# Optimization experiments

Measured on AMD Instinct MI355X. Metric: run time of the kernel, lower is better.

Reference implementation:

```python
import jax, jax.numpy as jnp
import numpy as np

N_CLASSES = 10
NBD_PAD = 1
EPS = 1e-5  # nn.LayerNorm default eps


def _neighbor_states(state, n):
    # state: [B, n_classes, H, W]; replicates F.unfold(kernel=2n+1, padding=n)
    # then drops the center tap. Kernel positions enumerated row-major, matching
    # unfold's (C, K2) channel ordering after the view in the torch code.
    B, C, H, W = state.shape
    k = 2 * n + 1
    center = (k * k) // 2
    padded = jnp.pad(state, ((0, 0), (0, 0), (n, n), (n, n)))
    shifts = []
    for idx in range(k * k):
        if idx == center:
            continue
        ki, kj = divmod(idx, k)
        shifts.append(padded[:, :, ki:ki + H, kj:kj + W])
    nb = jnp.stack(shifts, axis=2)  # [B, C, K2-1, H, W]
    return nb.reshape(B, C * (k * k - 1), H, W)


def setup_inputs() -> dict:
    key = jax.random.key(0)
    ks = jax.random.split(key, 7)
    B, C, H, W = 64, 32, 128, 128
    NN_HID, PERC = 128, 112
    x = jax.random.normal(ks[0], (B, C, H, W), dtype=jnp.float32)
    w1 = jax.random.normal(ks[1], (NN_HID, PERC), dtype=jnp.float32) * (1.0 / np.sqrt(PERC))
    b1 = jax.random.normal(ks[2], (NN_HID,), dtype=jnp.float32) * 0.02
    w2 = jax.random.normal(ks[3], (C, NN_HID), dtype=jnp.float32) * (1.0 / np.sqrt(NN_HID))
    b2 = jax.random.normal(ks[4], (C,), dtype=jnp.float32) * 0.02
    gamma = jnp.ones((C,), dtype=jnp.float32) + 0.1 * jax.random.normal(ks[5], (C,), dtype=jnp.float32)
    beta = 0.1 * jax.random.normal(ks[6], (C,), dtype=jnp.float32)
    return {"x": x, "w1": w1, "b1": b1, "w2": w2, "b2": b2, "gamma": gamma, "beta": beta}


def reference(x, w1, b1, w2, b2, gamma, beta):
    # perceive: [B, in_ch + n_classes*(K2-1), H, W]
    nb = _neighbor_states(x[:, :N_CLASSES], NBD_PAD)
    perc = jnp.concatenate([x, nb], axis=1)
    # 1x1 conv MLP (fire_rate == 1.0 -> no update mask)
    h = jax.nn.relu(jnp.einsum('bchw,oc->bohw', perc, w1) + b1[None, :, None, None])
    dx = jnp.einsum('bchw,oc->bohw', h, w2) + b2[None, :, None, None]
    new_state = x + dx
    # clean_slate_if_white: zero hidden channels where argmax class == 0 (no_grad mask)
    pred = jnp.argmax(new_state[:, :N_CLASSES], axis=1)  # [B,H,W]
    inv = jax.lax.stop_gradient((pred != 0).astype(new_state.dtype))[:, None]  # [B,1,H,W]
    new_state = jnp.concatenate(
        [new_state[:, :N_CLASSES], new_state[:, N_CLASSES:] * inv], axis=1)
    # LayerNorm over channel dim (torch permutes to NHWC, norms last dim, permutes back)
    mu = jnp.mean(new_state, axis=1, keepdims=True)
    var = jnp.var(new_state, axis=1, keepdims=True)
    xn = (new_state - mu) * jax.lax.rsqrt(var + EPS)
    return xn * gamma[None, :, None, None] + beta[None, :, None, None]
```

## Files before the change

kernel.cpp:

```cpp
#include <hip/hip_runtime.h>

typedef unsigned short U16;
typedef unsigned int U32;
typedef __bf16 bf16;
typedef bf16 bf16x8 __attribute__((ext_vector_type(8)));
typedef U16  u16x8  __attribute__((ext_vector_type(8)));
typedef float f32x4 __attribute__((ext_vector_type(4)));

__device__ __forceinline__ void split3(float a, U16& o1, U16& o2, U16& o3) {
    U32 ua = __float_as_uint(a);
    float a1 = __uint_as_float(ua & 0xFFFF0000u);
    float r1 = a - a1;
    U32 u2 = __float_as_uint(r1);
    float a2 = __uint_as_float(u2 & 0xFFFF0000u);
    float r2 = r1 - a2;
    o1 = (U16)(ua >> 16);
    o2 = (U16)(u2 >> 16);
    o3 = (U16)(__float_as_uint(r2) >> 16);
}

__device__ __forceinline__ void split3x8(const float v[8], bf16x8& A1, bf16x8& A2, bf16x8& A3) {
    u16x8 e1, e2, e3;
    #pragma unroll
    for (int j = 0; j < 8; ++j) { U16 a, b, c; split3(v[j], a, b, c); e1[j] = a; e2[j] = b; e3[j] = c; }
    A1 = __builtin_bit_cast(bf16x8, e1);
    A2 = __builtin_bit_cast(bf16x8, e2);
    A3 = __builtin_bit_cast(bf16x8, e3);
}

__global__ __launch_bounds__(256)
void prep_kernel(const float* __restrict__ w1g, const float* __restrict__ w2g,
                 U16* __restrict__ w1L, U16* __restrict__ w2L)
{
    int tid = blockIdx.x * 256 + threadIdx.x;
    if (tid < 2048) {
        int n = tid >> 4, k0 = (tid & 15) << 3;
        float v[8];
        #pragma unroll
        for (int j = 0; j < 8; ++j) { int k = k0 + j; v[j] = (k < 112) ? w1g[n * 112 + k] : 0.0f; }
        bf16x8 L1, L2, L3; split3x8(v, L1, L2, L3);
        *(bf16x8*)(w1L + 0 * 16384 + n * 128 + k0) = L1;
        *(bf16x8*)(w1L + 1 * 16384 + n * 128 + k0) = L2;
        *(bf16x8*)(w1L + 2 * 16384 + n * 128 + k0) = L3;
    }
    if (tid < 512) {
        int n = tid >> 4, k0 = (tid & 15) << 3;
        float v[8];
        #pragma unroll
        for (int j = 0; j < 8; ++j) v[j] = w2g[n * 128 + k0 + j];
        bf16x8 L1, L2, L3; split3x8(v, L1, L2, L3);
        *(bf16x8*)(w2L + 0 * 4096 + n * 128 + k0) = L1;
        *(bf16x8*)(w2L + 1 * 4096 + n * 128 + k0) = L2;
        *(bf16x8*)(w2L + 2 * 4096 + n * 128 + k0) = L3;
    }
}

#define WBAR() do { asm volatile("s_waitcnt lgkmcnt(0)" ::: "memory"); \
                    __builtin_amdgcn_s_barrier();                      \
                    asm volatile("" ::: "memory"); } while (0)
#define RBAR() do { asm volatile("" ::: "memory");                     \
                    __builtin_amdgcn_s_barrier();                      \
                    asm volatile("" ::: "memory"); } while (0)

__device__ __forceinline__ void tap_load(const float* __restrict__ xg, int b, int irow,
                                         int jbase, int j, float v[8])
{
    int tpx = j & 63, cls = j >> 6;
    const float* cbase = xg + (b * 32 + cls) * 16384;
    #pragma unroll
    for (int t = 0; t < 8; ++t) {
        int di = (int)((0x22211000u >> (4 * t)) & 0xFu) - 1;
        int dj = (int)((0x21020210u >> (4 * t)) & 0xFu) - 1;
        int row = irow + di;
        int cc  = jbase + tpx + dj;
        bool okb = ((unsigned)row < 128u) && ((unsigned)cc < 128u);
        int off = okb ? (row * 128 + cc) : 0;
        float x = cbase[off];
        v[t] = okb ? x : 0.0f;
    }
}

__device__ __forceinline__ void tap_write(U16* sL, int j, const float v[8])
{
    int tpx = j & 63, cls = j >> 6;
    bf16x8 T1, T2, T3; split3x8(v, T1, T2, T3);
    int to = tpx * 136 + 32 + cls * 8;
    *(bf16x8*)&sL[to] = T1;
    *(bf16x8*)&sL[8704 + to] = T2;
    *(bf16x8*)&sL[17408 + to] = T3;
}

#define LDW1(g, ks_) do {                                                    \
    _Pragma("unroll") for (int L_ = 0; L_ < 3; ++L_)                         \
    _Pragma("unroll") for (int n_ = 0; n_ < 2; ++n_)                         \
        g[L_ * 2 + n_] = *(const bf16x8*)(w1p + L_ * 16384 + n_ * 2048 + (ks_) * 32); \
} while (0)

#define MFMA1(ks_, g) do {                                                   \
    _Pragma("unroll") for (int mt_ = 0; mt_ < 4; ++mt_) {                    \
        const int ao_ = (mt_ * 16 + col) * 136 + (ks_) * 32 + quad * 8;      \
        bf16x8 A1_ = *(const bf16x8*)&sL[ao_];                               \
        bf16x8 A2_ = *(const bf16x8*)&sL[8704 + ao_];                        \
        bf16x8 A3_ = *(const bf16x8*)&sL[17408 + ao_];                       \
        _Pragma("unroll") for (int n_ = 0; n_ < 2; ++n_) {                   \
            f32x4 a_ = acc1[mt_][n_];                                        \
            a_ = __builtin_amdgcn_mfma_f32_16x16x32_bf16(A1_, g[0 + n_], a_, 0, 0, 0); \
            a_ = __builtin_amdgcn_mfma_f32_16x16x32_bf16(A1_, g[2 + n_], a_, 0, 0, 0); \
            a_ = __builtin_amdgcn_mfma_f32_16x16x32_bf16(A2_, g[0 + n_], a_, 0, 0, 0); \
            a_ = __builtin_amdgcn_mfma_f32_16x16x32_bf16(A1_, g[4 + n_], a_, 0, 0, 0); \
            a_ = __builtin_amdgcn_mfma_f32_16x16x32_bf16(A2_, g[2 + n_], a_, 0, 0, 0); \
            a_ = __builtin_amdgcn_mfma_f32_16x16x32_bf16(A3_, g[0 + n_], a_, 0, 0, 0); \
            acc1[mt_][n_] = a_;                                              \
        }                                                                    \
    }                                                                        \
} while (0)

#define LDW2(q, ks_) do {                                                    \
    _Pragma("unroll") for (int L_ = 0; L_ < 3; ++L_)                         \
    _Pragma("unroll") for (int n_ = 0; n_ < 2; ++n_)                         \
        q[L_ * 2 + n_] = *(const bf16x8*)(w2p + L_ * 4096 + n_ * 2048 + (ks_) * 32); \
} while (0)

#define MFMA2(ks_, q) do {                                                   \
    const int ho_ = (wv * 16 + col) * 136 + (ks_) * 32 + quad * 8;           \
    bf16x8 H1_ = *(const bf16x8*)&sL[ho_];                                   \
    bf16x8 H2_ = *(const bf16x8*)&sL[8704 + ho_];                            \
    bf16x8 H3_ = *(const bf16x8*)&sL[17408 + ho_];                           \
    _Pragma("unroll") for (int n_ = 0; n_ < 2; ++n_) {                       \
        f32x4 a_ = acc2[n_];                                                 \
        a_ = __builtin_amdgcn_mfma_f32_16x16x32_bf16(H1_, q[0 + n_], a_, 0, 0, 0); \
        a_ = __builtin_amdgcn_mfma_f32_16x16x32_bf16(H1_, q[2 + n_], a_, 0, 0, 0); \
        a_ = __builtin_amdgcn_mfma_f32_16x16x32_bf16(H2_, q[0 + n_], a_, 0, 0, 0); \
        a_ = __builtin_amdgcn_mfma_f32_16x16x32_bf16(H1_, q[4 + n_], a_, 0, 0, 0); \
        a_ = __builtin_amdgcn_mfma_f32_16x16x32_bf16(H2_, q[2 + n_], a_, 0, 0, 0); \
        a_ = __builtin_amdgcn_mfma_f32_16x16x32_bf16(H3_, q[0 + n_], a_, 0, 0, 0); \
        acc2[n_] = a_;                                                       \
    }                                                                        \
} while (0)

__global__ __launch_bounds__(256, 3)
void cann_kernel(const float* __restrict__ xg,  const U16* __restrict__ w1L,
                 const U16* __restrict__ w2L,
                 const float* __restrict__ b1g, const float* __restrict__ b2g,
                 const float* __restrict__ gg,  const float* __restrict__ bg,
                 float* __restrict__ outg)
{
    __shared__ __align__(16) U16 sL[3 * 8704];

    const int tid  = threadIdx.x;
    const int bid0 = blockIdx.x;
    const int bid  = (bid0 & 7) * 2048 + (bid0 >> 3);
    const int jseg = bid & 1;
    const int irow = (bid >> 1) & 127;
    const int b    = bid >> 8;
    const int jbase = jseg << 6;
    const int lane = tid & 63;
    const int wv   = tid >> 6;
    const int quad = lane >> 4;
    const int col  = lane & 15;
    const int px   = tid & 63;
    const int cg   = tid >> 6;

    const U16* w1p = w1L + (wv * 32 + col) * 128 + quad * 8;
    const U16* w2p = w2L + col * 128 + quad * 8;

    {
        const float* src = xg + (b * 32 + cg * 8) * 16384 + irow * 128 + jbase + px;
        float va[8];
        #pragma unroll
        for (int i = 0; i < 8; ++i) va[i] = src[i * 16384];
        bf16x8 L1, L2, L3; split3x8(va, L1, L2, L3);
        int o = px * 136 + cg * 8;
        *(bf16x8*)&sL[o] = L1;
        *(bf16x8*)&sL[8704 + o] = L2;
        *(bf16x8*)&sL[17408 + o] = L3;
    }
    {
        float vt[8];
        tap_load(xg, b, irow, jbase, tid, vt);       tap_write(sL, tid, vt);
        tap_load(xg, b, irow, jbase, tid + 256, vt); tap_write(sL, tid + 256, vt);
        if (tid < 128) { tap_load(xg, b, irow, jbase, tid + 512, vt);
                         tap_write(sL, tid + 512, vt); }
    }
    if (tid < 128) {
        int zo = (tid >> 1) * 136 + 112 + (tid & 1) * 8;
        uint4 z = make_uint4(0u, 0u, 0u, 0u);
        *(uint4*)&sL[zo] = z;
        *(uint4*)&sL[8704 + zo] = z;
        *(uint4*)&sL[17408 + zo] = z;
    }

    const float b1v0 = b1g[wv * 32 + col];
    const float b1v1 = b1g[wv * 32 + 16 + col];
    const float b2v0 = b2g[col];
    const float b2v1 = b2g[16 + col];
    float xs[2][4];
    #pragma unroll
    for (int n2 = 0; n2 < 2; ++n2)
        #pragma unroll
        for (int r = 0; r < 4; ++r)
            xs[n2][r] = xg[(b * 32 + n2 * 16 + col) * 16384 + irow * 128 + jbase
                           + wv * 16 + quad * 4 + r];

    bf16x8 g0[6], g1[6], g2[6], g3[6];
    LDW1(g0, 0);
    LDW1(g1, 1);

    WBAR();

    const f32x4 fz = {0.f, 0.f, 0.f, 0.f};
    f32x4 acc1[4][2];
    #pragma unroll
    for (int mt = 0; mt < 4; ++mt) { acc1[mt][0] = fz; acc1[mt][1] = fz; }

    LDW1(g2, 2);
    __builtin_amdgcn_sched_group_barrier(0x20, 6, 0);
    MFMA1(0, g0);
    LDW1(g3, 3);
    __builtin_amdgcn_sched_group_barrier(0x20, 6, 0);
    MFMA1(1, g1);
    MFMA1(2, g2);
    MFMA1(3, g3);

    RBAR();

    bf16x8 q0[6], q1[6], q2[6], q3[6];
    LDW2(q0, 0);
    LDW2(q1, 1);
    __builtin_amdgcn_sched_group_barrier(0x20, 12, 0);

    #pragma unroll
    for (int mt = 0; mt < 4; ++mt)
        #pragma unroll
        for (int n2 = 0; n2 < 2; ++n2) {
            float bb = n2 ? b1v1 : b1v0;
            #pragma unroll
            for (int r = 0; r < 4; ++r) {
                float v = fmaxf(acc1[mt][n2][r] + bb, 0.0f);
                U16 u1, u2, u3; split3(v, u1, u2, u3);
                int ho = (mt * 16 + quad * 4 + r) * 136 + wv * 32 + n2 * 16 + col;
                sL[ho] = u1; sL[8704 + ho] = u2; sL[17408 + ho] = u3;
            }
        }

    WBAR();

    f32x4 acc2[2];
    acc2[0] = fz; acc2[1] = fz;

    LDW2(q2, 2);
    __builtin_amdgcn_sched_group_barrier(0x20, 6, 0);
    MFMA2(0, q0);
    LDW2(q3, 3);
    __builtin_amdgcn_sched_group_barrier(0x20, 6, 0);
    MFMA2(1, q1);
    MFMA2(2, q2);
    MFMA2(3, q3);

    RBAR();

    float* dxl = (float*)sL;
    #pragma unroll
    for (int n2 = 0; n2 < 2; ++n2) {
        float bb = n2 ? b2v1 : b2v0;
        int c = n2 * 16 + col;
        #pragma unroll
        for (int r = 0; r < 4; ++r) {
            int p = wv * 16 + quad * 4 + r;
            dxl[p * 33 + c] = acc2[n2][r] + bb + xs[n2][r];
        }
    }

    WBAR();

    if (tid < 64) {
        int p = tid;
        float ns[32];
        #pragma unroll
        for (int c = 0; c < 32; ++c) ns[c] = dxl[p * 33 + c];
        float m = ns[1];
        #pragma unroll
        for (int c = 2; c < 10; ++c) m = fmaxf(m, ns[c]);
        float keep = (m > ns[0]) ? 1.0f : 0.0f;
        #pragma unroll
        for (int c = 10; c < 32; ++c) ns[c] *= keep;
        float s = 0.f;
        #pragma unroll
        for (int c = 0; c < 32; ++c) s += ns[c];
        float mu = s * 0.03125f;
        float var = 0.f;
        #pragma unroll
        for (int c = 0; c < 32; ++c) { float d = ns[c] - mu; var += d * d; }
        var *= 0.03125f;
        float rstd = 1.0f / sqrtf(var + 1e-5f);
        int base = b * 524288 + irow * 128 + jbase + p;
        #pragma unroll
        for (int c = 0; c < 32; ++c)
            outg[base + c * 16384] = (ns[c] - mu) * rstd * gg[c] + bg[c];
    }
}

extern "C" void kernel_launch(void* const* d_in, const int* in_sizes, int n_in,
                              void* d_out, int out_size, void* d_ws, size_t ws_size,
                              hipStream_t stream) {
    const float* x  = (const float*)d_in[0];
    const float* w1 = (const float*)d_in[1];
    const float* b1 = (const float*)d_in[2];
    const float* w2 = (const float*)d_in[3];
    const float* b2 = (const float*)d_in[4];
    const float* g  = (const float*)d_in[5];
    const float* be = (const float*)d_in[6];
    float* out = (float*)d_out;

    U16* w1L = (U16*)d_ws;
    U16* w2L = (U16*)((char*)d_ws + 98304);

    hipLaunchKernelGGL(prep_kernel, dim3(8), dim3(256), 0, stream, w1, w2, w1L, w2L);
    hipLaunchKernelGGL(cann_kernel, dim3(16384), dim3(256), 0, stream,
                       x, w1L, w2L, b1, b2, g, be, out);
}
```

Measured before the change: 578.0 us.

## Process two 64-pixel tiles per block and prefetch the second tile's inputs

Each block now handles a full 128-pixel row as two tiles, halving the grid. The global loads for the second tile are issued during the first tile's second GEMM so their latency overlaps compute. The MFMA operands are swapped, which transposes the accumulator layout and allows vectorized u16x4 stores of the hidden activations and f32x4 stores into a padded dx buffer. In exchange the prefetch buffers raise register pressure, and the grid has less parallelism to hide latency.

```diff
diff --git a/kernel.cpp b/kernel.cpp
--- a/kernel.cpp
+++ b/kernel.cpp
@@ -5,6 +5,7 @@
 typedef __bf16 bf16;
 typedef bf16 bf16x8 __attribute__((ext_vector_type(8)));
 typedef U16  u16x8  __attribute__((ext_vector_type(8)));
+typedef U16  u16x4  __attribute__((ext_vector_type(4)));
 typedef float f32x4 __attribute__((ext_vector_type(4)));
 
 __device__ __forceinline__ void split3(float a, U16& o1, U16& o2, U16& o3) {
@@ -90,13 +91,62 @@
     *(bf16x8*)&sL[17408 + to] = T3;
 }
 
+__device__ __forceinline__ void load_tile(const float* __restrict__ xg, int b, int irow,
+                                          int jbase, int tid, int px, int cg,
+                                          int wv, int quad, int col,
+                                          float va[8], float vt0[8], float vt1[8],
+                                          float vt2[8], float xs[2][4])
+{
+    const float* src = xg + (b * 32 + cg * 8) * 16384 + irow * 128 + jbase + px;
+    #pragma unroll
+    for (int i = 0; i < 8; ++i) va[i] = src[i * 16384];
+    tap_load(xg, b, irow, jbase, tid,       vt0);
+    tap_load(xg, b, irow, jbase, tid + 256, vt1);
+    if (tid < 128) tap_load(xg, b, irow, jbase, tid + 512, vt2);
+    #pragma unroll
+    for (int n2 = 0; n2 < 2; ++n2)
+        #pragma unroll
+        for (int r = 0; r < 4; ++r)
+            xs[n2][r] = xg[(b * 32 + n2 * 16 + quad * 4 + r) * 16384
+                           + irow * 128 + jbase + wv * 16 + col];
+}
+
+__device__ __forceinline__ void stage_all(U16* sL, int tid, int px, int cg,
+                                          const float va[8], const float vt0[8],
+                                          const float vt1[8], const float vt2[8])
+{
+    {
+        bf16x8 L1, L2, L3; split3x8(va, L1, L2, L3);
+        int o = px * 136 + cg * 8;
+        *(bf16x8*)&sL[o] = L1;
+        *(bf16x8*)&sL[8704 + o] = L2;
+        *(bf16x8*)&sL[17408 + o] = L3;
+    }
+    tap_write(sL, tid,       vt0);
+    tap_write(sL, tid + 256, vt1);
+    if (tid < 128) tap_write(sL, tid + 512, vt2);
+    if (tid < 128) {
+        int zo = (tid >> 1) * 136 + 112 + (tid & 1) * 8;
+        uint4 z = make_uint4(0u, 0u, 0u, 0u);
+        *(uint4*)&sL[zo] = z;
+        *(uint4*)&sL[8704 + zo] = z;
+        *(uint4*)&sL[17408 + zo] = z;
+    }
+}
+
 #define LDW1(g, ks_) do {                                                    \
     _Pragma("unroll") for (int L_ = 0; L_ < 3; ++L_)                         \
     _Pragma("unroll") for (int n_ = 0; n_ < 2; ++n_)                         \
         g[L_ * 2 + n_] = *(const bf16x8*)(w1p + L_ * 16384 + n_ * 2048 + (ks_) * 32); \
 } while (0)
 
-#define MFMA1(ks_, g) do {                                                   \
+#define LDW2(q, ks_) do {                                                    \
+    _Pragma("unroll") for (int L_ = 0; L_ < 3; ++L_)                         \
+    _Pragma("unroll") for (int n_ = 0; n_ < 2; ++n_)                         \
+        q[L_ * 2 + n_] = *(const bf16x8*)(w2p + L_ * 4096 + n_ * 2048 + (ks_) * 32); \
+} while (0)
+
+#define MFMA1S(ks_, g) do {                                                  \
     _Pragma("unroll") for (int mt_ = 0; mt_ < 4; ++mt_) {                    \
         const int ao_ = (mt_ * 16 + col) * 136 + (ks_) * 32 + quad * 8;      \
         bf16x8 A1_ = *(const bf16x8*)&sL[ao_];                               \
@@ -104,38 +154,149 @@
         bf16x8 A3_ = *(const bf16x8*)&sL[17408 + ao_];                       \
         _Pragma("unroll") for (int n_ = 0; n_ < 2; ++n_) {                   \
             f32x4 a_ = acc1[mt_][n_];                                        \
-            a_ = __builtin_amdgcn_mfma_f32_16x16x32_bf16(A1_, g[0 + n_], a_, 0, 0, 0); \
-            a_ = __builtin_amdgcn_mfma_f32_16x16x32_bf16(A1_, g[2 + n_], a_, 0, 0, 0); \
-            a_ = __builtin_amdgcn_mfma_f32_16x16x32_bf16(A2_, g[0 + n_], a_, 0, 0, 0); \
-            a_ = __builtin_amdgcn_mfma_f32_16x16x32_bf16(A1_, g[4 + n_], a_, 0, 0, 0); \
-            a_ = __builtin_amdgcn_mfma_f32_16x16x32_bf16(A2_, g[2 + n_], a_, 0, 0, 0); \
-            a_ = __builtin_amdgcn_mfma_f32_16x16x32_bf16(A3_, g[0 + n_], a_, 0, 0, 0); \
+            a_ = __builtin_amdgcn_mfma_f32_16x16x32_bf16(g[0 + n_], A1_, a_, 0, 0, 0); \
+            a_ = __builtin_amdgcn_mfma_f32_16x16x32_bf16(g[2 + n_], A1_, a_, 0, 0, 0); \
+            a_ = __builtin_amdgcn_mfma_f32_16x16x32_bf16(g[0 + n_], A2_, a_, 0, 0, 0); \
+            a_ = __builtin_amdgcn_mfma_f32_16x16x32_bf16(g[4 + n_], A1_, a_, 0, 0, 0); \
+            a_ = __builtin_amdgcn_mfma_f32_16x16x32_bf16(g[2 + n_], A2_, a_, 0, 0, 0); \
+            a_ = __builtin_amdgcn_mfma_f32_16x16x32_bf16(g[0 + n_], A3_, a_, 0, 0, 0); \
             acc1[mt_][n_] = a_;                                              \
         }                                                                    \
     }                                                                        \
 } while (0)
 
-#define LDW2(q, ks_) do {                                                    \
-    _Pragma("unroll") for (int L_ = 0; L_ < 3; ++L_)                         \
-    _Pragma("unroll") for (int n_ = 0; n_ < 2; ++n_)                         \
-        q[L_ * 2 + n_] = *(const bf16x8*)(w2p + L_ * 4096 + n_ * 2048 + (ks_) * 32); \
-} while (0)
-
-#define MFMA2(ks_, q) do {                                                   \
+#define MFMA2S(ks_, q) do {                                                  \
     const int ho_ = (wv * 16 + col) * 136 + (ks_) * 32 + quad * 8;           \
     bf16x8 H1_ = *(const bf16x8*)&sL[ho_];                                   \
     bf16x8 H2_ = *(const bf16x8*)&sL[8704 + ho_];                            \
     bf16x8 H3_ = *(const bf16x8*)&sL[17408 + ho_];                           \
     _Pragma("unroll") for (int n_ = 0; n_ < 2; ++n_) {                       \
         f32x4 a_ = acc2[n_];                                                 \
-        a_ = __builtin_amdgcn_mfma_f32_16x16x32_bf16(H1_, q[0 + n_], a_, 0, 0, 0); \
-        a_ = __builtin_amdgcn_mfma_f32_16x16x32_bf16(H1_, q[2 + n_], a_, 0, 0, 0); \
-        a_ = __builtin_amdgcn_mfma_f32_16x16x32_bf16(H2_, q[0 + n_], a_, 0, 0, 0); \
-        a_ = __builtin_amdgcn_mfma_f32_16x16x32_bf16(H1_, q[4 + n_], a_, 0, 0, 0); \
-        a_ = __builtin_amdgcn_mfma_f32_16x16x32_bf16(H2_, q[2 + n_], a_, 0, 0, 0); \
-        a_ = __builtin_amdgcn_mfma_f32_16x16x32_bf16(H3_, q[0 + n_], a_, 0, 0, 0); \
+        a_ = __builtin_amdgcn_mfma_f32_16x16x32_bf16(q[0 + n_], H1_, a_, 0, 0, 0); \
+        a_ = __builtin_amdgcn_mfma_f32_16x16x32_bf16(q[2 + n_], H1_, a_, 0, 0, 0); \
+        a_ = __builtin_amdgcn_mfma_f32_16x16x32_bf16(q[0 + n_], H2_, a_, 0, 0, 0); \
+        a_ = __builtin_amdgcn_mfma_f32_16x16x32_bf16(q[4 + n_], H1_, a_, 0, 0, 0); \
+        a_ = __builtin_amdgcn_mfma_f32_16x16x32_bf16(q[2 + n_], H2_, a_, 0, 0, 0); \
+        a_ = __builtin_amdgcn_mfma_f32_16x16x32_bf16(q[0 + n_], H3_, a_, 0, 0, 0); \
         acc2[n_] = a_;                                                       \
     }                                                                        \
+} while (0)
+
+#define EPI3(jb_) do {                                                       \
+    const float* dxr_ = (const float*)sL;                                    \
+    int p_ = tid;                                                            \
+    f32x4 e0_ = *(const f32x4*)&dxr_[p_ * 36 + 0];                           \
+    f32x4 e1_ = *(const f32x4*)&dxr_[p_ * 36 + 4];                           \
+    f32x4 e2_ = *(const f32x4*)&dxr_[p_ * 36 + 8];                           \
+    float m_ = e0_[1];                                                       \
+    m_ = fmaxf(m_, e0_[2]); m_ = fmaxf(m_, e0_[3]);                          \
+    m_ = fmaxf(m_, e1_[0]); m_ = fmaxf(m_, e1_[1]);                          \
+    m_ = fmaxf(m_, e1_[2]); m_ = fmaxf(m_, e1_[3]);                          \
+    m_ = fmaxf(m_, e2_[0]); m_ = fmaxf(m_, e2_[1]);                          \
+    float keep_ = (m_ > e0_[0]) ? 1.0f : 0.0f;                               \
+    float s_ = 0.f;                                                          \
+    s_ += e0_[0]; s_ += e0_[1]; s_ += e0_[2]; s_ += e0_[3];                  \
+    s_ += e1_[0]; s_ += e1_[1]; s_ += e1_[2]; s_ += e1_[3];                  \
+    s_ += e2_[0]; s_ += e2_[1];                                              \
+    s_ += e2_[2] * keep_; s_ += e2_[3] * keep_;                              \
+    _Pragma("unroll")                                                        \
+    for (int i_ = 3; i_ < 8; ++i_) {                                         \
+        f32x4 v_ = *(const f32x4*)&dxr_[p_ * 36 + i_ * 4];                   \
+        s_ += v_[0] * keep_; s_ += v_[1] * keep_;                            \
+        s_ += v_[2] * keep_; s_ += v_[3] * keep_;                            \
+    }                                                                        \
+    float mu_ = s_ * 0.03125f;                                               \
+    float var_ = 0.f;                                                        \
+    _Pragma("unroll")                                                        \
+    for (int i_ = 0; i_ < 8; ++i_) {                                         \
+        f32x4 v_ = *(const f32x4*)&dxr_[p_ * 36 + i_ * 4];                   \
+        _Pragma("unroll")                                                    \
+        for (int j_ = 0; j_ < 4; ++j_) {                                     \
+            int c_ = i_ * 4 + j_;                                            \
+            float x_ = (c_ >= 10) ? v_[j_] * keep_ : v_[j_];                 \
+            float d_ = x_ - mu_; var_ += d_ * d_;                            \
+        }                                                                    \
+    }                                                                        \
+    var_ *= 0.03125f;                                                        \
+    float rstd_ = 1.0f / sqrtf(var_ + 1e-5f);                                \
+    int base_ = b * 524288 + irow * 128 + (jb_) + p_;                        \
+    _Pragma("unroll")                                                        \
+    for (int i_ = 0; i_ < 8; ++i_) {                                         \
+        f32x4 v_ = *(const f32x4*)&dxr_[p_ * 36 + i_ * 4];                   \
+        _Pragma("unroll")                                                    \
+        for (int j_ = 0; j_ < 4; ++j_) {                                     \
+            int c_ = i_ * 4 + j_;                                            \
+            float x_ = (c_ >= 10) ? v_[j_] * keep_ : v_[j_];                 \
+            outg[base_ + c_ * 16384] = (x_ - mu_) * rstd_ * gg[c_] + bg[c_]; \
+        }                                                                    \
+    }                                                                        \
+} while (0)
+
+#define TILE_BODY(jb_, XS_, PRE_, jb2_, XSN_) do {                           \
+    stage_all(sL, tid, px, cg, va, vt0, vt1, vt2);                           \
+    bf16x8 g0[6], g1[6], g2[6], g3[6];                                       \
+    LDW1(g0, 0); LDW1(g1, 1);                                                \
+    WBAR();             \
+    f32x4 acc1[4][2];                                                        \
+    _Pragma("unroll")                                                        \
+    for (int mt_ = 0; mt_ < 4; ++mt_) { acc1[mt_][0] = fz; acc1[mt_][1] = fz; } \
+    LDW1(g2, 2);                                                             \
+    __builtin_amdgcn_sched_group_barrier(0x20, 6, 0);                        \
+    MFMA1S(0, g0);                                                           \
+    LDW1(g3, 3);                                                             \
+    __builtin_amdgcn_sched_group_barrier(0x20, 6, 0);                        \
+    MFMA1S(1, g1);                                                           \
+    MFMA1S(2, g2);                                                           \
+    MFMA1S(3, g3);                                                           \
+    RBAR();            \
+    bf16x8 q0[6], q1[6], q2[6], q3[6];                                       \
+    LDW2(q0, 0); LDW2(q1, 1);                                                \
+    __builtin_amdgcn_sched_group_barrier(0x20, 12, 0);                       \
+     \
+    _Pragma("unroll")                                                        \
+    for (int mt_ = 0; mt_ < 4; ++mt_)                                        \
+        _Pragma("unroll")                                                    \
+        for (int n_ = 0; n_ < 2; ++n_) {                                     \
+            u16x4 o1_, o2_, o3_;                                             \
+            _Pragma("unroll")                                                \
+            for (int r_ = 0; r_ < 4; ++r_) {                                 \
+                float v_ = fmaxf(acc1[mt_][n_][r_] + b1v[n_][r_], 0.0f);     \
+                U16 u1_, u2_, u3_; split3(v_, u1_, u2_, u3_);                \
+                o1_[r_] = u1_; o2_[r_] = u2_; o3_[r_] = u3_;                 \
+            }                                                                \
+            int ho_ = (mt_ * 16 + col) * 136 + wv * 32 + n_ * 16 + quad * 4; \
+            *(u16x4*)&sL[ho_] = o1_;                                         \
+            *(u16x4*)&sL[8704 + ho_] = o2_;                                  \
+            *(u16x4*)&sL[17408 + ho_] = o3_;                                 \
+        }                                                                    \
+    WBAR();                                      \
+    if (PRE_) load_tile(xg, b, irow, (jb2_), tid, px, cg, wv, quad, col,     \
+                        va, vt0, vt1, vt2, XSN_);                            \
+    f32x4 acc2[2];                                                           \
+    acc2[0] = fz; acc2[1] = fz;                                              \
+    LDW2(q2, 2);                                                             \
+    __builtin_amdgcn_sched_group_barrier(0x20, 6, 0);                        \
+    MFMA2S(0, q0);                                                           \
+    LDW2(q3, 3);                                                             \
+    __builtin_amdgcn_sched_group_barrier(0x20, 6, 0);                        \
+    MFMA2S(1, q1);                                                           \
+    MFMA2S(2, q2);                                                           \
+    MFMA2S(3, q3);                                                           \
+    RBAR();         \
+    {        \
+        float* dxl_ = (float*)sL;                                            \
+        _Pragma("unroll")                                                    \
+        for (int n_ = 0; n_ < 2; ++n_) {                                     \
+            f32x4 vv_;                                                       \
+            _Pragma("unroll")                                                \
+            for (int r_ = 0; r_ < 4; ++r_)                                   \
+                vv_[r_] = acc2[n_][r_] + b2v[n_][r_] + XS_[n_][r_];          \
+            *(f32x4*)&dxl_[(wv * 16 + col) * 36 + n_ * 16 + quad * 4] = vv_; \
+        }                                                                    \
+    }                                                                        \
+    WBAR();                                      \
+    if (tid < 64) EPI3(jb_);                                                 \
+    if (PRE_) WBAR();   \
 } while (0)
 
 __global__ __launch_bounds__(256, 3)
@@ -149,11 +310,9 @@
 
     const int tid  = threadIdx.x;
     const int bid0 = blockIdx.x;
-    const int bid  = (bid0 & 7) * 2048 + (bid0 >> 3);
-    const int jseg = bid & 1;
-    const int irow = (bid >> 1) & 127;
-    const int b    = bid >> 8;
-    const int jbase = jseg << 6;
+    const int bid  = (bid0 & 7) * 1024 + (bid0 >> 3);
+    const int irow = bid & 127;
+    const int b    = bid >> 7;
     const int lane = tid & 63;
     const int wv   = tid >> 6;
     const int quad = lane >> 4;
@@ -164,140 +323,22 @@
     const U16* w1p = w1L + (wv * 32 + col) * 128 + quad * 8;
     const U16* w2p = w2L + col * 128 + quad * 8;
 
-    {
-        const float* src = xg + (b * 32 + cg * 8) * 16384 + irow * 128 + jbase + px;
-        float va[8];
-        #pragma unroll
-        for (int i = 0; i < 8; ++i) va[i] = src[i * 16384];
-        bf16x8 L1, L2, L3; split3x8(va, L1, L2, L3);
-        int o = px * 136 + cg * 8;
-        *(bf16x8*)&sL[o] = L1;
-        *(bf16x8*)&sL[8704 + o] = L2;
-        *(bf16x8*)&sL[17408 + o] = L3;
-    }
-    {
-        float vt[8];
-        tap_load(xg, b, irow, jbase, tid, vt);       tap_write(sL, tid, vt);
-        tap_load(xg, b, irow, jbase, tid + 256, vt); tap_write(sL, tid + 256, vt);
-        if (tid < 128) { tap_load(xg, b, irow, jbase, tid + 512, vt);
-                         tap_write(sL, tid + 512, vt); }
-    }
-    if (tid < 128) {
-        int zo = (tid >> 1) * 136 + 112 + (tid & 1) * 8;
-        uint4 z = make_uint4(0u, 0u, 0u, 0u);
-        *(uint4*)&sL[zo] = z;
-        *(uint4*)&sL[8704 + zo] = z;
-        *(uint4*)&sL[17408 + zo] = z;
-    }
-
-    const float b1v0 = b1g[wv * 32 + col];
-    const float b1v1 = b1g[wv * 32 + 16 + col];
-    const float b2v0 = b2g[col];
-    const float b2v1 = b2g[16 + col];
-    float xs[2][4];
+    float b1v[2][4], b2v[2][4];
     #pragma unroll
     for (int n2 = 0; n2 < 2; ++n2)
         #pragma unroll
-        for (int r = 0; r < 4; ++r)
-            xs[n2][r] = xg[(b * 32 + n2 * 16 + col) * 16384 + irow * 128 + jbase
-                           + wv * 16 + quad * 4 + r];
-
-    bf16x8 g0[6], g1[6], g2[6], g3[6];
-    LDW1(g0, 0);
-    LDW1(g1, 1);
-
-    WBAR();
+        for (int r = 0; r < 4; ++r) {
+            b1v[n2][r] = b1g[wv * 32 + n2 * 16 + quad * 4 + r];
+            b2v[n2][r] = b2g[n2 * 16 + quad * 4 + r];
+        }
 
     const f32x4 fz = {0.f, 0.f, 0.f, 0.f};
-    f32x4 acc1[4][2];
-    #pragma unroll
-    for (int mt = 0; mt < 4; ++mt) { acc1[mt][0] = fz; acc1[mt][1] = fz; }
-
-    LDW1(g2, 2);
-    __builtin_amdgcn_sched_group_barrier(0x20, 6, 0);
-    MFMA1(0, g0);
-    LDW1(g3, 3);
-    __builtin_amdgcn_sched_group_barrier(0x20, 6, 0);
-    MFMA1(1, g1);
-    MFMA1(2, g2);
-    MFMA1(3, g3);
-
-    RBAR();
-
-    bf16x8 q0[6], q1[6], q2[6], q3[6];
-    LDW2(q0, 0);
-    LDW2(q1, 1);
-    __builtin_amdgcn_sched_group_barrier(0x20, 12, 0);
-
-    #pragma unroll
-    for (int mt = 0; mt < 4; ++mt)
-        #pragma unroll
-        for (int n2 = 0; n2 < 2; ++n2) {
-            float bb = n2 ? b1v1 : b1v0;
-            #pragma unroll
-            for (int r = 0; r < 4; ++r) {
-                float v = fmaxf(acc1[mt][n2][r] + bb, 0.0f);
-                U16 u1, u2, u3; split3(v, u1, u2, u3);
-                int ho = (mt * 16 + quad * 4 + r) * 136 + wv * 32 + n2 * 16 + col;
-                sL[ho] = u1; sL[8704 + ho] = u2; sL[17408 + ho] = u3;
-            }
-        }
-
-    WBAR();
-
-    f32x4 acc2[2];
-    acc2[0] = fz; acc2[1] = fz;
-
-    LDW2(q2, 2);
-    __builtin_amdgcn_sched_group_barrier(0x20, 6, 0);
-    MFMA2(0, q0);
-    LDW2(q3, 3);
-    __builtin_amdgcn_sched_group_barrier(0x20, 6, 0);
-    MFMA2(1, q1);
-    MFMA2(2, q2);
-    MFMA2(3, q3);
-
-    RBAR();
-
-    float* dxl = (float*)sL;
-    #pragma unroll
-    for (int n2 = 0; n2 < 2; ++n2) {
-        float bb = n2 ? b2v1 : b2v0;
-        int c = n2 * 16 + col;
-        #pragma unroll
-        for (int r = 0; r < 4; ++r) {
-            int p = wv * 16 + quad * 4 + r;
-            dxl[p * 33 + c] = acc2[n2][r] + bb + xs[n2][r];
-        }
-    }
-
-    WBAR();
-
-    if (tid < 64) {
-        int p = tid;
-        float ns[32];
-        #pragma unroll
-        for (int c = 0; c < 32; ++c) ns[c] = dxl[p * 33 + c];
-        float m = ns[1];
-        #pragma unroll
-        for (int c = 2; c < 10; ++c) m = fmaxf(m, ns[c]);
-        float keep = (m > ns[0]) ? 1.0f : 0.0f;
-        #pragma unroll
-        for (int c = 10; c < 32; ++c) ns[c] *= keep;
-        float s = 0.f;
-        #pragma unroll
-        for (int c = 0; c < 32; ++c) s += ns[c];
-        float mu = s * 0.03125f;
-        float var = 0.f;
-        #pragma unroll
-        for (int c = 0; c < 32; ++c) { float d = ns[c] - mu; var += d * d; }
-        var *= 0.03125f;
-        float rstd = 1.0f / sqrtf(var + 1e-5f);
-        int base = b * 524288 + irow * 128 + jbase + p;
-        #pragma unroll
-        for (int c = 0; c < 32; ++c)
-            outg[base + c * 16384] = (ns[c] - mu) * rstd * gg[c] + bg[c];
-    }
+
+    float va[8], vt0[8], vt1[8], vt2[8], xsA[2][4], xsB[2][4];
+    load_tile(xg, b, irow, 0, tid, px, cg, wv, quad, col, va, vt0, vt1, vt2, xsA);
+
+    TILE_BODY(0,  xsA, 1, 64, xsB);
+    TILE_BODY(64, xsB, 0, 0,  xsA);
 }
 
 extern "C" void kernel_launch(void* const* d_in, const int* in_sizes, int n_in,
@@ -316,6 +357,6 @@
     U16* w2L = (U16*)((char*)d_ws + 98304);
 
     hipLaunchKernelGGL(prep_kernel, dim3(8), dim3(256), 0, stream, w1, w2, w1L, w2L);
-    hipLaunchKernelGGL(cann_kernel, dim3(16384), dim3(256), 0, stream,
+    hipLaunchKernelGGL(cann_kernel, dim3(8192), dim3(256), 0, stream,
                        x, w1L, w2L, b1, b2, g, be, out);
 }
```

Result: slower. 685.7 us (+18.6%).
